# Optimization experiments

Measured on AMD Instinct MI355X. Metric: run time of the kernel, lower is better.

Reference implementation:

```python
import jax, jax.numpy as jnp
import numpy as np

MD = 4       # max displacement per level (md=[4,...] in VCN)
WSIZE = 3    # truncation window half-size in flow_reg


def _corrf(ref, tar, md=MD):
    """VCN.corrf: per-channel shifted-product 4D cost volume + leaky_relu.
    cost[b,c,i,j,y,x] = leaky_relu(ref[b,c,y,x] * tar[b,c,y+(j-md), x+(i-md)], 0.1)
    (zero outside valid region, matching the torch zero-filled buffer)."""
    B, C, H, W = ref.shape
    U = 2 * md + 1
    tar_pad = jnp.pad(tar, ((0, 0), (0, 0), (md, md), (md, md)))
    # dim 2 ordered as i*U + j (i = x-shift index, j = y-shift index)
    shifts = jnp.stack([tar_pad[:, :, j:j + H, i:i + W]
                        for i in range(U) for j in range(U)], axis=2)
    cost = jax.nn.leaky_relu(ref[:, :, None] * shifts, 0.1)
    return cost.reshape(B, C, U, U, H, W)


def _flow_reg(x, md=MD, wsize=WSIZE):
    """flow_reg with ent=True: argmax -> 7x7 box mask over (u,v) (the MaxPool3d on a
    one-hot scatter is exactly a Chebyshev-box around the argmax) -> masked softmax
    over u*v -> soft-argmax flow + local/global entropies."""
    B, U, V, H, W = x.shape
    idx = jnp.argmax(x.reshape(B, U * V, H, W), axis=1)         # (B,H,W)
    ub, vb = idx // V, idx % V
    uu = jnp.arange(U)[None, :, None, None, None]
    vv = jnp.arange(V)[None, None, :, None, None]
    mask = (jnp.abs(uu - ub[:, None, None]) <= wsize) & \
           (jnp.abs(vv - vb[:, None, None]) <= wsize)           # (B,U,V,H,W)
    neg_inf = jnp.array(-jnp.inf, x.dtype)
    p = jax.nn.softmax(jnp.where(mask, x, neg_inf).reshape(B, U * V, H, W),
                       axis=1).reshape(B, U, V, H, W)
    fx = (jnp.arange(U) - md).astype(x.dtype)[None, :, None, None, None]
    fy = (jnp.arange(V) - md).astype(x.dtype)[None, None, :, None, None]
    outx = jnp.sum(p * fx, axis=(1, 2))[:, None]                # (B,1,H,W)
    outy = jnp.sum(p * fy, axis=(1, 2))[:, None]
    def _ent(q):
        return (-q * jnp.log(jnp.clip(q, 1e-9, 1 - 1e-9))).sum(axis=(1, 2))[:, None]
    local_ent = _ent(p) / np.log((2 * wsize + 1) ** 2).astype(np.float32)
    pg = jax.nn.softmax(x.reshape(B, U * V, H, W), axis=1).reshape(B, U, V, H, W)
    global_ent = _ent(pg) / np.log(U * V).astype(np.float32)
    return jnp.concatenate([outx, outy], 1), jnp.concatenate([local_ent, global_ent], 1)


def _warp(x, flo):
    """grid_sample-based backward warp (bilinear, zero padding, align_corners=True)
    plus the in-bounds mask, exactly as VCN's warp()."""
    B, C, H, W = x.shape
    px = jnp.arange(W, dtype=flo.dtype)[None, None, :] + flo[:, 0]   # (B,H,W)
    py = jnp.arange(H, dtype=flo.dtype)[None, :, None] + flo[:, 1]
    inb = (jnp.abs(2.0 * px / max(W - 1, 1) - 1.0) < 1) & \
          (jnp.abs(2.0 * py / max(H - 1, 1) - 1.0) < 1)
    x0 = jnp.floor(px); y0 = jnp.floor(py)
    wx = px - x0; wy = py - y0
    x0i = x0.astype(jnp.int32); y0i = y0.astype(jnp.int32)
    flat = x.reshape(B, C, H * W)
    def tap(yi, xi, wgt):
        valid = (xi >= 0) & (xi < W) & (yi >= 0) & (yi < H)
        lin = jnp.clip(yi, 0, H - 1) * W + jnp.clip(xi, 0, W - 1)
        v = jax.vmap(lambda img, l: img[:, l])(flat, lin)            # (B,C,H,W)
        return v * (wgt * valid.astype(x.dtype))[:, None]
    out = (tap(y0i,     x0i,     (1 - wx) * (1 - wy)) +
           tap(y0i,     x0i + 1, wx * (1 - wy)) +
           tap(y0i + 1, x0i,     (1 - wx) * wy) +
           tap(y0i + 1, x0i + 1, wx * wy))
    return out * inb.astype(x.dtype)[:, None], inb


def setup_inputs() -> dict:
    key = jax.random.key(0)
    k1, k2, k3 = jax.random.split(key, 3)
    B, C, H, W, F = 2, 128, 64, 64, 16
    ref = jax.random.normal(k1, (B, C, H, W), jnp.float32) * 0.5
    tar = jax.random.normal(k2, (B, C, H, W), jnp.float32) * 0.5
    pw = jax.random.normal(k3, (F, C), jnp.float32) / np.sqrt(C).astype(np.float32)
    return {"ref_feat": ref, "tar_feat": tar, "proj_w": pw}


def reference(ref_feat, tar_feat, proj_w):
    B, C, H, W = ref_feat.shape
    F_ = proj_w.shape[0]
    U = 2 * MD + 1
    cost = _corrf(ref_feat, tar_feat)                       # (B,C,U,U,H,W)
    # 1x1 channel contraction of the 4D cost volume (butterfly4D input proj)
    cvol = jnp.einsum('bcuvhw,fc->bfuvhw', cost, proj_w)    # (B,F,U,U,H,W)
    flow_h, ent_h = _flow_reg(cvol.reshape(B * F_, U, U, H, W))
    flow = flow_h.reshape(B, F_, 2, H, W)[:, 0]             # first hypothesis
    warped, _ = _warp(tar_feat, flow)
    return jnp.concatenate([flow_h, ent_h], axis=1), warped
```

## Files before the change

### kernel.cpp

```cpp
#include <hip/hip_runtime.h>
#include <math.h>

#define B_ 2
#define C_ 128
#define H_ 64
#define W_ 64
#define F_ 16
#define U_ 9
#define MD_ 4
#define UV_ 81
#define HW_ (H_*W_)
#define BF_ (B_*F_)

typedef float f32x4 __attribute__((ext_vector_type(4)));
typedef float f32x2 __attribute__((ext_vector_type(2)));
typedef _Float16 f16x2 __attribute__((ext_vector_type(2)));
typedef _Float16 f16x4 __attribute__((ext_vector_type(4)));
typedef _Float16 f16x8 __attribute__((ext_vector_type(8)));

#define XSCALE   64.0f
#define WSCALE   256.0f
#define UNSCALE  (1.0f / 16384.0f)

#define TARS 42
#define REFO 12096
#define SM_  11016
#define SI_  11528
#define SU_  12040
#define LDSZ 15112

static __device__ __forceinline__ f16x8 cat4(f16x2 a, f16x2 b, f16x2 c, f16x2 d) {
    f16x4 ab = __builtin_shufflevector(a, b, 0, 1, 2, 3);
    f16x4 cd = __builtin_shufflevector(c, d, 0, 1, 2, 3);
    return __builtin_shufflevector(ab, cd, 0, 1, 2, 3, 4, 5, 6, 7);
}

static __device__ __forceinline__ void split2(f32x2 p, f16x2& hi, f16x2& lo) {
    hi = __builtin_bit_cast(f16x2, __builtin_amdgcn_cvt_pkrtz(p.x, p.y));
    f32x2 hf; hf.x = (float)hi.x; hf.y = (float)hi.y;
    f32x2 l = p - hf;
    lo = __builtin_bit_cast(f16x2, __builtin_amdgcn_cvt_pkrtz(l.x, l.y));
}

__global__ __launch_bounds__(512, 2)
void fused_kernel(const float* __restrict__ ref,
                  const float* __restrict__ tar,
                  const float* __restrict__ pw,
                  float* __restrict__ out0) {
    const int t    = threadIdx.x;
    const int lane = t & 63;
    const int wid  = t >> 6;
    const int xt   = wid & 1;
    const int uvg  = wid >> 1;
    const int ml   = lane & 15;
    const int grp  = lane >> 4;
    const int pxl  = xt * 16 + ml;

    const int n0 = blockIdx.x;
    const int L  = (n0 & 7) * 32 + (n0 >> 3);
    const int b  = L >> 7;
    const int y  = (L >> 1) & 63;
    const int xh = L & 1;
    const int x0 = xh * 32;

    const int start = (uvg == 0) ? 0 : (1 + uvg * 20);

    __shared__ float lds[LDSZ];

    const float* refB = ref + ((size_t)b * C_) * HW_ + y * W_ + x0;
    const float* tarB = tar + ((size_t)b * C_) * HW_;

    int uA[21], vA[21];
    #pragma unroll
    for (int i = 0; i < 21; ++i) {
        int uv = start + i;
        int uu = uv / 9;
        uA[i] = uu; vA[i] = uv - uu * 9;
    }

    float nstg[23], nref[2];

#define SISSUE(KC) {                                                          \
    _Pragma("unroll")                                                         \
    for (int it = 0; it < 23; ++it) {                                         \
        int idx = it * 512 + t;                                               \
        int seg = idx / 40;                                                   \
        int col = idx - seg * 40;                                             \
        int c   = seg / 9;                                                    \
        int r   = seg - c * 9;                                                \
        int cc  = c > 31 ? 31 : c;                                            \
        int ysr = y + r - 4;                                                  \
        int xg  = x0 - 4 + col;                                               \
        bool ok = (it < 22 || t < 256) &&                                     \
                  ((unsigned)ysr < 64u) && ((unsigned)xg < 64u);              \
        int ysc = ysr < 0 ? 0 : (ysr > 63 ? 63 : ysr);                        \
        int xgc = xg  < 0 ? 0 : (xg  > 63 ? 63 : xg);                         \
        float vL = tarB[(size_t)((KC) * 32 + cc) * HW_ + ysc * W_ + xgc];     \
        nstg[it] = ok ? vL : 0.f;                                             \
    }                                                                         \
    _Pragma("unroll")                                                         \
    for (int it = 0; it < 2; ++it) {                                          \
        int idx = it * 512 + t;                                               \
        nref[it] = refB[(size_t)((KC) * 32 + (idx >> 5)) * HW_ + (idx & 31)]; \
    } }

#define SWRITE() {                                                            \
    _Pragma("unroll")                                                         \
    for (int it = 0; it < 23; ++it) {                                         \
        int idx = it * 512 + t;                                               \
        if (it < 22 || t < 256) {                                             \
            int seg = idx / 40;                                               \
            int col = idx - seg * 40;                                         \
            lds[seg * TARS + col] = nstg[it];                                 \
        }                                                                     \
    }                                                                         \
    _Pragma("unroll")                                                         \
    for (int it = 0; it < 2; ++it) {                                          \
        int idx = it * 512 + t;                                               \
        lds[REFO + idx] = nref[it] * XSCALE;                                  \
    } }

    f32x4 acc[21];
    #pragma unroll
    for (int i = 0; i < 21; ++i) acc[i] = f32x4{0.f, 0.f, 0.f, 0.f};

    SISSUE(0);

    for (int kc = 0; kc < 4; ++kc) {
        f32x4 wa = *(const f32x4*)(pw + ml * C_ + kc * 32 + grp * 8);
        f32x4 wb = *(const f32x4*)(pw + ml * C_ + kc * 32 + grp * 8 + 4);

        __syncthreads();
        SWRITE();
        if (kc < 3) SISSUE(kc + 1);
        __syncthreads();

        f16x2 wh[4], wl[4];
        {
            f32x2 p;
            p.x = wa.x * WSCALE; p.y = wa.y * WSCALE; split2(p, wh[0], wl[0]);
            p.x = wa.z * WSCALE; p.y = wa.w * WSCALE; split2(p, wh[1], wl[1]);
            p.x = wb.x * WSCALE; p.y = wb.y * WSCALE; split2(p, wh[2], wl[2]);
            p.x = wb.z * WSCALE; p.y = wb.w * WSCALE; split2(p, wh[3], wl[3]);
        }
        f16x8 whi = cat4(wh[0], wh[1], wh[2], wh[3]);
        f16x8 wlo = cat4(wl[0], wl[1], wl[2], wl[3]);

        float rv[8];
        #pragma unroll
        for (int j = 0; j < 8; ++j)
            rv[j] = lds[REFO + (grp * 8 + j) * 32 + pxl];

        const int rowbase = grp * 8 * (9 * TARS);

#define UVBODY(i) {                                                           \
        const int cb = vA[i] * TARS + pxl + uA[i];                            \
        f16x2 xh4[4], xl4[4];                                                 \
        _Pragma("unroll")                                                     \
        for (int jp = 0; jp < 4; ++jp) {                                      \
            float t0 = lds[rowbase + (2 * jp    ) * (9 * TARS) + cb];         \
            float t1 = lds[rowbase + (2 * jp + 1) * (9 * TARS) + cb];         \
            f32x2 p;  p.x = rv[2 * jp] * t0;  p.y = rv[2 * jp + 1] * t1;      \
            f32x2 p1 = p * 0.1f;                                              \
            p = __builtin_elementwise_max(p, p1);                             \
            split2(p, xh4[jp], xl4[jp]);                                      \
        }                                                                     \
        f16x8 xhi = cat4(xh4[0], xh4[1], xh4[2], xh4[3]);                     \
        f16x8 xlo = cat4(xl4[0], xl4[1], xl4[2], xl4[3]);                     \
        acc[i] = __builtin_amdgcn_mfma_f32_16x16x32_f16(whi, xhi, acc[i], 0, 0, 0); \
        acc[i] = __builtin_amdgcn_mfma_f32_16x16x32_f16(wlo, xhi, acc[i], 0, 0, 0); \
        acc[i] = __builtin_amdgcn_mfma_f32_16x16x32_f16(whi, xlo, acc[i], 0, 0, 0); }

        #pragma unroll
        for (int i = 0; i < 20; ++i) UVBODY(i);
        if (uvg == 0) UVBODY(20);
    }
    __syncthreads();

    const int jw  = t >> 7;
    const int rem = t & 127;
    const int fl  = rem >> 5;
    const int px  = rem & 31;

#define PH1(S0, N) {                                                          \
    _Pragma("unroll")                                                         \
    for (int i = 0; i < (N); ++i)                                             \
        vv[i] = lds[(fl * 81 + (S0) + i) * 34 + px];                          \
    mv = vv[0]; bi = (S0);                                                    \
    _Pragma("unroll")                                                         \
    for (int i = 1; i < (N); ++i)                                             \
        if (vv[i] > mv) { mv = vv[i]; bi = (S0) + i; } }

#define PH2(S0, N) {                                                          \
    _Pragma("unroll")                                                         \
    for (int i = 0; i < (N); ++i) {                                           \
        const int uvx = (S0) + i;                                             \
        const int uu = uvx / 9, vy = uvx - 9 * (uvx / 9);                     \
        float d = vv[i] - m; float z = __expf(d);                             \
        gS += z; gA = fmaf(z, d, gA);                                         \
        int duc = uu - ub, dvc = vy - vb;                                     \
        bool msk = (duc <= 3) && (duc >= -3) && (dvc <= 3) && (dvc >= -3);    \
        float zm = msk ? z : 0.f, dm = msk ? d : 0.f;                         \
        S += zm; A = fmaf(zm, dm, A);                                         \
        Sx = fmaf(zm, (float)(uu - MD_), Sx);                                 \
        Sy = fmaf(zm, (float)(vy - MD_), Sy); } }

    for (int P = 0; P < 4; ++P) {
#define BOUNCE(i) {                                                           \
        int uvx = start + (i);                                                \
        if (grp == P) {                                                       \
            lds[(0 * 81 + uvx) * 34 + pxl] = acc[i][0] * UNSCALE;             \
            lds[(1 * 81 + uvx) * 34 + pxl] = acc[i][1] * UNSCALE;             \
            lds[(2 * 81 + uvx) * 34 + pxl] = acc[i][2] * UNSCALE;             \
            lds[(3 * 81 + uvx) * 34 + pxl] = acc[i][3] * UNSCALE; } }
        #pragma unroll
        for (int i = 0; i < 20; ++i) BOUNCE(i);
        if (uvg == 0) BOUNCE(20);
        __syncthreads();

        float vv[21]; float mv; int bi;
        if      (jw == 0) { PH1(0, 21) }
        else if (jw == 1) { PH1(21, 20) }
        else if (jw == 2) { PH1(41, 20) }
        else              { PH1(61, 20) }
        lds[SM_ + t] = mv; lds[SI_ + t] = (float)bi;
        __syncthreads();

        float m = lds[SM_ + rem]; int best = (int)lds[SI_ + rem];
        #pragma unroll
        for (int k = 1; k < 4; ++k) {
            float mk = lds[SM_ + rem + 128 * k];
            if (mk > m) { m = mk; best = (int)lds[SI_ + rem + 128 * k]; }
        }
        int ub = best / 9, vb = best - 9 * (best / 9);

        float S = 0.f, A = 0.f, Sx = 0.f, Sy = 0.f, gS = 0.f, gA = 0.f;
        if      (jw == 0) { PH2(0, 21) }
        else if (jw == 1) { PH2(21, 20) }
        else if (jw == 2) { PH2(41, 20) }
        else              { PH2(61, 20) }
        lds[SU_ + 0 * 512 + t] = S;  lds[SU_ + 1 * 512 + t] = A;
        lds[SU_ + 2 * 512 + t] = Sx; lds[SU_ + 3 * 512 + t] = Sy;
        lds[SU_ + 4 * 512 + t] = gS; lds[SU_ + 5 * 512 + t] = gA;
        __syncthreads();

        if (t < 128) {
            float rq[6];
            #pragma unroll
            for (int q = 0; q < 6; ++q) {
                float s = lds[SU_ + q * 512 + t];
                #pragma unroll
                for (int k = 1; k < 4; ++k) s += lds[SU_ + q * 512 + t + 128 * k];
                rq[q] = s;
            }
            float invS = 1.f / rq[0];
            float outx = rq[2] * invS;
            float outy = rq[3] * invS;
            float lent = (logf(rq[0]) - rq[1] * invS) * (1.0f / logf(49.0f));
            float gent = (logf(rq[4]) - rq[5] / rq[4]) * (1.0f / logf(81.0f));
            float* op = out0 + ((size_t)(b * F_ + P * 4 + fl) * 4) * HW_
                      + y * W_ + x0 + px;
            op[0 * HW_] = outx;
            op[1 * HW_] = outy;
            op[2 * HW_] = lent;
            op[3 * HW_] = gent;
        }
        __syncthreads();
    }
}

__global__ __launch_bounds__(256)
void warp_kernel(const float* __restrict__ tar,
                 const float* __restrict__ out0,
                 float* __restrict__ warped) {
    int tid = blockIdx.x * 256 + threadIdx.x;
    int pix = tid & (HW_ - 1);
    int bc  = tid >> 12;
    int b   = bc >> 7;
    int x = pix & 63, y = pix >> 6;

    const float* fbase = out0 + (size_t)(b * F_) * 4 * HW_;
    float fx = fbase[pix];
    float fy = fbase[HW_ + pix];
    float px = (float)x + fx;
    float py = (float)y + fy;

    bool inb = (fabsf(2.0f * px / (float)(W_ - 1) - 1.0f) < 1.0f) &&
               (fabsf(2.0f * py / (float)(H_ - 1) - 1.0f) < 1.0f);

    float x0 = floorf(px), y0 = floorf(py);
    float wx = px - x0,    wy = py - y0;
    int x0i = (int)x0, y0i = (int)y0;

    const float* img = tar + (size_t)bc * HW_;

    auto tap = [&](int yi, int xi, float wgt) -> float {
        bool v = ((unsigned)xi < (unsigned)W_) && ((unsigned)yi < (unsigned)H_);
        int xc = xi < 0 ? 0 : (xi > W_ - 1 ? W_ - 1 : xi);
        int yc = yi < 0 ? 0 : (yi > H_ - 1 ? H_ - 1 : yi);
        float val = img[yc * W_ + xc];
        return val * (v ? wgt : 0.f);
    };

    float acc = tap(y0i,     x0i,     (1.f - wx) * (1.f - wy))
              + tap(y0i,     x0i + 1, wx * (1.f - wy))
              + tap(y0i + 1, x0i,     (1.f - wx) * wy)
              + tap(y0i + 1, x0i + 1, wx * wy);

    warped[tid] = inb ? acc : 0.f;
}

extern "C" void kernel_launch(void* const* d_in, const int* in_sizes, int n_in,
                              void* d_out, int out_size, void* d_ws, size_t ws_size,
                              hipStream_t stream) {
    const float* ref = (const float*)d_in[0];
    const float* tar = (const float*)d_in[1];
    const float* pw  = (const float*)d_in[2];
    float* out0 = (float*)d_out;
    float* out1 = out0 + (size_t)BF_ * 4 * HW_;
    (void)d_ws; (void)ws_size;

    fused_kernel<<<256, 512, 0, stream>>>(ref, tar, pw, out0);
    warp_kernel<<<(B_ * C_ * HW_) / 256, 256, 0, stream>>>(tar, out0, out1);
}
```

Before: 105.1 us.

## Halve pixel tile per block and transpose LDS layout for vector reads

Each block now covers 16 pixels instead of 32, so the grid doubles to 512 blocks. Each of the 8 waves owns about 10 uv shifts rather than splitting by pixel half. The target and ref tiles are stored channel-contiguous in LDS, so each lane fetches 8 channels with two 128-bit loads instead of strided scalar loads. Ref is loaded once up front and launch bounds ask for 4 blocks per CU; this trades more blocks and more halo overlap in the target tile for better occupancy and fewer registers per thread.

Result: slower. 131.7 us (+25.4%).

```diff
diff --git a/kernel.cpp b/kernel.cpp
--- a/kernel.cpp
+++ b/kernel.cpp
@@ -22,12 +22,12 @@
 #define WSCALE   256.0f
 #define UNSCALE  (1.0f / 16384.0f)
 
-#define TARS 42
-#define REFO 12096
-#define SM_  11016
-#define SI_  11528
-#define SU_  12040
-#define LDSZ 15112
+#define TARB 0
+#define REFO 7776
+#define SM_  9888
+#define SI_  10400
+#define SU_  10912
+#define LDSZ 13984
 
 static __device__ __forceinline__ f16x8 cat4(f16x2 a, f16x2 b, f16x2 c, f16x2 d) {
     f16x4 ab = __builtin_shufflevector(a, b, 0, 1, 2, 3);
@@ -42,7 +42,7 @@
     lo = __builtin_bit_cast(f16x2, __builtin_amdgcn_cvt_pkrtz(l.x, l.y));
 }
 
-__global__ __launch_bounds__(512, 2)
+__global__ __launch_bounds__(512, 4)
 void fused_kernel(const float* __restrict__ ref,
                   const float* __restrict__ tar,
                   const float* __restrict__ pw,
@@ -50,79 +50,71 @@
     const int t    = threadIdx.x;
     const int lane = t & 63;
     const int wid  = t >> 6;
-    const int xt   = wid & 1;
-    const int uvg  = wid >> 1;
     const int ml   = lane & 15;
     const int grp  = lane >> 4;
-    const int pxl  = xt * 16 + ml;
 
     const int n0 = blockIdx.x;
-    const int L  = (n0 & 7) * 32 + (n0 >> 3);
-    const int b  = L >> 7;
-    const int y  = (L >> 1) & 63;
-    const int xh = L & 1;
-    const int x0 = xh * 32;
-
-    const int start = (uvg == 0) ? 0 : (1 + uvg * 20);
+    const int L  = (n0 & 7) * 64 + (n0 >> 3);
+    const int b  = L >> 8;
+    const int y  = (L >> 2) & 63;
+    const int xq = L & 3;
+    const int x0 = xq * 16;
+
+    const int start = wid ? (1 + wid * 10) : 0;
 
     __shared__ float lds[LDSZ];
 
     const float* refB = ref + ((size_t)b * C_) * HW_ + y * W_ + x0;
     const float* tarB = tar + ((size_t)b * C_) * HW_;
 
-    int uA[21], vA[21];
+    int uA[11], vA[11];
     #pragma unroll
-    for (int i = 0; i < 21; ++i) {
+    for (int i = 0; i < 11; ++i) {
         int uv = start + i;
         int uu = uv / 9;
         uA[i] = uu; vA[i] = uv - uu * 9;
     }
 
-    float nstg[23], nref[2];
-
+    #pragma unroll
+    for (int it = 0; it < 4; ++it) {
+        int idx = it * 512 + t;
+        int c = idx >> 4, px = idx & 15;
+        lds[REFO + px * 132 + c] = refB[(size_t)c * HW_ + px] * XSCALE;
+    }
+
+    float nstg[14];
 #define SISSUE(KC) {                                                          \
     _Pragma("unroll")                                                         \
-    for (int it = 0; it < 23; ++it) {                                         \
+    for (int it = 0; it < 14; ++it) {                                         \
         int idx = it * 512 + t;                                               \
-        int seg = idx / 40;                                                   \
-        int col = idx - seg * 40;                                             \
-        int c   = seg / 9;                                                    \
-        int r   = seg - c * 9;                                                \
-        int cc  = c > 31 ? 31 : c;                                            \
+        int c0  = idx / 216;                                                  \
+        int rem = idx - c0 * 216;                                             \
+        int r   = rem / 24;                                                   \
+        int col = rem - r * 24;                                               \
         int ysr = y + r - 4;                                                  \
         int xg  = x0 - 4 + col;                                               \
-        bool ok = (it < 22 || t < 256) &&                                     \
-                  ((unsigned)ysr < 64u) && ((unsigned)xg < 64u);              \
+        bool ok = (idx < 6912) && ((unsigned)ysr < 64u) && ((unsigned)xg < 64u); \
+        int cc  = c0 > 31 ? 31 : c0;                                          \
         int ysc = ysr < 0 ? 0 : (ysr > 63 ? 63 : ysr);                        \
         int xgc = xg  < 0 ? 0 : (xg  > 63 ? 63 : xg);                         \
         float vL = tarB[(size_t)((KC) * 32 + cc) * HW_ + ysc * W_ + xgc];     \
         nstg[it] = ok ? vL : 0.f;                                             \
-    }                                                                         \
-    _Pragma("unroll")                                                         \
-    for (int it = 0; it < 2; ++it) {                                          \
-        int idx = it * 512 + t;                                               \
-        nref[it] = refB[(size_t)((KC) * 32 + (idx >> 5)) * HW_ + (idx & 31)]; \
     } }
 
 #define SWRITE() {                                                            \
     _Pragma("unroll")                                                         \
-    for (int it = 0; it < 23; ++it) {                                         \
+    for (int it = 0; it < 14; ++it) {                                         \
         int idx = it * 512 + t;                                               \
-        if (it < 22 || t < 256) {                                             \
-            int seg = idx / 40;                                               \
-            int col = idx - seg * 40;                                         \
-            lds[seg * TARS + col] = nstg[it];                                 \
+        if (idx < 6912) {                                                     \
+            int c0  = idx / 216;                                              \
+            int rem = idx - c0 * 216;                                         \
+            lds[rem * 36 + c0] = nstg[it];                                    \
         }                                                                     \
-    }                                                                         \
-    _Pragma("unroll")                                                         \
-    for (int it = 0; it < 2; ++it) {                                          \
-        int idx = it * 512 + t;                                               \
-        lds[REFO + idx] = nref[it] * XSCALE;                                  \
     } }
 
-    f32x4 acc[21];
+    f32x4 acc[11];
     #pragma unroll
-    for (int i = 0; i < 21; ++i) acc[i] = f32x4{0.f, 0.f, 0.f, 0.f};
+    for (int i = 0; i < 11; ++i) acc[i] = f32x4{0.f, 0.f, 0.f, 0.f};
 
     SISSUE(0);
 
@@ -146,21 +138,20 @@
         f16x8 whi = cat4(wh[0], wh[1], wh[2], wh[3]);
         f16x8 wlo = cat4(wl[0], wl[1], wl[2], wl[3]);
 
-        float rv[8];
-        #pragma unroll
-        for (int j = 0; j < 8; ++j)
-            rv[j] = lds[REFO + (grp * 8 + j) * 32 + pxl];
-
-        const int rowbase = grp * 8 * (9 * TARS);
+        f32x4 rva = *(const f32x4*)(lds + REFO + ml * 132 + kc * 32 + grp * 8);
+        f32x4 rvb = *(const f32x4*)(lds + REFO + ml * 132 + kc * 32 + grp * 8 + 4);
+        float rv[8] = {rva.x, rva.y, rva.z, rva.w, rvb.x, rvb.y, rvb.z, rvb.w};
 
 #define UVBODY(i) {                                                           \
-        const int cb = vA[i] * TARS + pxl + uA[i];                            \
+        const int cb = (vA[i] * 24 + ml + uA[i]) * 36 + grp * 8;              \
+        f32x4 ta = *(const f32x4*)(lds + cb);                                 \
+        f32x4 tb = *(const f32x4*)(lds + cb + 4);                             \
+        float t8[8] = {ta.x, ta.y, ta.z, ta.w, tb.x, tb.y, tb.z, tb.w};       \
         f16x2 xh4[4], xl4[4];                                                 \
         _Pragma("unroll")                                                     \
         for (int jp = 0; jp < 4; ++jp) {                                      \
-            float t0 = lds[rowbase + (2 * jp    ) * (9 * TARS) + cb];         \
-            float t1 = lds[rowbase + (2 * jp + 1) * (9 * TARS) + cb];         \
-            f32x2 p;  p.x = rv[2 * jp] * t0;  p.y = rv[2 * jp + 1] * t1;      \
+            f32x2 p;  p.x = rv[2 * jp] * t8[2 * jp];                          \
+                      p.y = rv[2 * jp + 1] * t8[2 * jp + 1];                  \
             f32x2 p1 = p * 0.1f;                                              \
             p = __builtin_elementwise_max(p, p1);                             \
             split2(p, xh4[jp], xl4[jp]);                                      \
@@ -172,85 +163,75 @@
         acc[i] = __builtin_amdgcn_mfma_f32_16x16x32_f16(whi, xlo, acc[i], 0, 0, 0); }
 
         #pragma unroll
-        for (int i = 0; i < 20; ++i) UVBODY(i);
-        if (uvg == 0) UVBODY(20);
+        for (int i = 0; i < 10; ++i) UVBODY(i);
+        if (wid == 0) UVBODY(10);
     }
     __syncthreads();
 
-    const int jw  = t >> 7;
-    const int rem = t & 127;
-    const int fl  = rem >> 5;
-    const int px  = rem & 31;
-
-#define PH1(S0, N) {                                                          \
-    _Pragma("unroll")                                                         \
-    for (int i = 0; i < (N); ++i)                                             \
-        vv[i] = lds[(fl * 81 + (S0) + i) * 34 + px];                          \
-    mv = vv[0]; bi = (S0);                                                    \
-    _Pragma("unroll")                                                         \
-    for (int i = 1; i < (N); ++i)                                             \
-        if (vv[i] > mv) { mv = vv[i]; bi = (S0) + i; } }
-
-#define PH2(S0, N) {                                                          \
-    _Pragma("unroll")                                                         \
-    for (int i = 0; i < (N); ++i) {                                           \
-        const int uvx = (S0) + i;                                             \
-        const int uu = uvx / 9, vy = uvx - 9 * (uvx / 9);                     \
+    const int rem = t & 63;
+    const int fl  = rem >> 4;
+    const int px  = rem & 15;
+
+    for (int P = 0; P < 4; ++P) {
+#define BOUNCE(i) {                                                           \
+        if (grp == P) {                                                       \
+            int ba = (start + (i)) * 18 + ml;                                 \
+            lds[ba         ] = acc[i][0] * UNSCALE;                           \
+            lds[ba + 1458  ] = acc[i][1] * UNSCALE;                           \
+            lds[ba + 2916  ] = acc[i][2] * UNSCALE;                           \
+            lds[ba + 4374  ] = acc[i][3] * UNSCALE; } }
+        #pragma unroll
+        for (int i = 0; i < 10; ++i) BOUNCE(i);
+        if (wid == 0) BOUNCE(10);
+        __syncthreads();
+
+        float vv[11];
+        #pragma unroll
+        for (int i = 0; i < 10; ++i)
+            vv[i] = lds[fl * 1458 + (start + i) * 18 + px];
+        if (wid == 0) vv[10] = lds[fl * 1458 + 10 * 18 + px];
+        float mv = vv[0]; int bi = start;
+        #pragma unroll
+        for (int i = 1; i < 10; ++i)
+            if (vv[i] > mv) { mv = vv[i]; bi = start + i; }
+        if (wid == 0 && vv[10] > mv) { mv = vv[10]; bi = 10; }
+        lds[SM_ + t] = mv; lds[SI_ + t] = (float)bi;
+        __syncthreads();
+
+        float m = lds[SM_ + rem]; int best = (int)lds[SI_ + rem];
+        #pragma unroll
+        for (int k = 1; k < 8; ++k) {
+            float mk = lds[SM_ + k * 64 + rem];
+            if (mk > m) { m = mk; best = (int)lds[SI_ + k * 64 + rem]; }
+        }
+        int ub = best / 9, vb = best - 9 * (best / 9);
+
+        float S = 0.f, A = 0.f, Sx = 0.f, Sy = 0.f, gS = 0.f, gA = 0.f;
+#define PH2B(i) {                                                             \
         float d = vv[i] - m; float z = __expf(d);                             \
         gS += z; gA = fmaf(z, d, gA);                                         \
-        int duc = uu - ub, dvc = vy - vb;                                     \
+        int duc = uA[i] - ub, dvc = vA[i] - vb;                               \
         bool msk = (duc <= 3) && (duc >= -3) && (dvc <= 3) && (dvc >= -3);    \
         float zm = msk ? z : 0.f, dm = msk ? d : 0.f;                         \
         S += zm; A = fmaf(zm, dm, A);                                         \
-        Sx = fmaf(zm, (float)(uu - MD_), Sx);                                 \
-        Sy = fmaf(zm, (float)(vy - MD_), Sy); } }
-
-    for (int P = 0; P < 4; ++P) {
-#define BOUNCE(i) {                                                           \
-        int uvx = start + (i);                                                \
-        if (grp == P) {                                                       \
-            lds[(0 * 81 + uvx) * 34 + pxl] = acc[i][0] * UNSCALE;             \
-            lds[(1 * 81 + uvx) * 34 + pxl] = acc[i][1] * UNSCALE;             \
-            lds[(2 * 81 + uvx) * 34 + pxl] = acc[i][2] * UNSCALE;             \
-            lds[(3 * 81 + uvx) * 34 + pxl] = acc[i][3] * UNSCALE; } }
-        #pragma unroll
-        for (int i = 0; i < 20; ++i) BOUNCE(i);
-        if (uvg == 0) BOUNCE(20);
-        __syncthreads();
-
-        float vv[21]; float mv; int bi;
-        if      (jw == 0) { PH1(0, 21) }
-        else if (jw == 1) { PH1(21, 20) }
-        else if (jw == 2) { PH1(41, 20) }
-        else              { PH1(61, 20) }
-        lds[SM_ + t] = mv; lds[SI_ + t] = (float)bi;
-        __syncthreads();
-
-        float m = lds[SM_ + rem]; int best = (int)lds[SI_ + rem];
-        #pragma unroll
-        for (int k = 1; k < 4; ++k) {
-            float mk = lds[SM_ + rem + 128 * k];
-            if (mk > m) { m = mk; best = (int)lds[SI_ + rem + 128 * k]; }
-        }
-        int ub = best / 9, vb = best - 9 * (best / 9);
-
-        float S = 0.f, A = 0.f, Sx = 0.f, Sy = 0.f, gS = 0.f, gA = 0.f;
-        if      (jw == 0) { PH2(0, 21) }
-        else if (jw == 1) { PH2(21, 20) }
-        else if (jw == 2) { PH2(41, 20) }
-        else              { PH2(61, 20) }
+        Sx = fmaf(zm, (float)(uA[i] - MD_), Sx);                              \
+        Sy = fmaf(zm, (float)(vA[i] - MD_), Sy); }
+        #pragma unroll
+        for (int i = 0; i < 10; ++i) PH2B(i);
+        if (wid == 0) PH2B(10);
+
         lds[SU_ + 0 * 512 + t] = S;  lds[SU_ + 1 * 512 + t] = A;
         lds[SU_ + 2 * 512 + t] = Sx; lds[SU_ + 3 * 512 + t] = Sy;
         lds[SU_ + 4 * 512 + t] = gS; lds[SU_ + 5 * 512 + t] = gA;
         __syncthreads();
 
-        if (t < 128) {
+        if (t < 64) {
             float rq[6];
             #pragma unroll
             for (int q = 0; q < 6; ++q) {
                 float s = lds[SU_ + q * 512 + t];
                 #pragma unroll
-                for (int k = 1; k < 4; ++k) s += lds[SU_ + q * 512 + t + 128 * k];
+                for (int k = 1; k < 8; ++k) s += lds[SU_ + q * 512 + k * 64 + t];
                 rq[q] = s;
             }
             float invS = 1.f / rq[0];
@@ -258,8 +239,8 @@
             float outy = rq[3] * invS;
             float lent = (logf(rq[0]) - rq[1] * invS) * (1.0f / logf(49.0f));
             float gent = (logf(rq[4]) - rq[5] / rq[4]) * (1.0f / logf(81.0f));
-            float* op = out0 + ((size_t)(b * F_ + P * 4 + fl) * 4) * HW_
-                      + y * W_ + x0 + px;
+            float* op = out0 + ((size_t)(b * F_ + P * 4 + (t >> 4)) * 4) * HW_
+                      + y * W_ + x0 + (t & 15);
             op[0 * HW_] = outx;
             op[1 * HW_] = outy;
             op[2 * HW_] = lent;
@@ -320,6 +301,6 @@
     float* out1 = out0 + (size_t)BF_ * 4 * HW_;
     (void)d_ws; (void)ws_size;
 
-    fused_kernel<<<256, 512, 0, stream>>>(ref, tar, pw, out0);
+    fused_kernel<<<512, 512, 0, stream>>>(ref, tar, pw, out0);
     warp_kernel<<<(B_ * C_ * HW_) / 256, 256, 0, stream>>>(tar, out0, out1);
 }
```
